# Optimization experiments

Measured on AMD Instinct MI355X. Metric: run time of the kernel, lower is better.

The kernel has to match this reference:

```python
import jax, jax.numpy as jnp
import numpy as np

EPS = 1e-6
SCALE = 1.0
GRID_HEIGHT = 4.0
GRID_RES_Y = 1.0


def _perspective(mat, vec):
    # mat [3,4], vec [...,3] -> (points [...,2], flag [...,3])
    homog = jnp.einsum('ij,...j->...i', mat[:, :3], vec) + mat[:, 3]
    pos = homog[..., 2:3] > 0
    flag = jnp.concatenate([pos, pos, jnp.ones_like(pos)], axis=-1).astype(homog.dtype)
    homog = homog * flag  # zero x,y behind camera; z kept (flag[...,-1]=True)
    return homog[..., :2] / homog[..., 2:3], flag


def _fisheye(pts, k, D, flag):
    cx, cy, fx, fy = k[0, 2], k[1, 2], k[0, 0], k[1, 1]
    x = (pts[..., 0] - cx) / fx
    y = (pts[..., 1] - cy) / fy
    r = jnp.sqrt(x * x + y * y)
    th = jnp.arctan(r)
    t2 = th * th
    rad = th * (1 + D[0] * t2 + D[1] * t2 ** 2 + D[2] * t2 ** 3 + D[5] * t2 ** 4) / r
    xd = x * rad * fx + cx
    yd = y * rad * fy + cy
    return jnp.stack([xd, yd], axis=-1) * flag[..., :2]


def _pinhole(pts, k, D, flag):
    cx, cy, fx, fy = k[0, 2], k[1, 2], k[0, 0], k[1, 1]
    x = (pts[..., 0] - cx) / fx
    y = (pts[..., 1] - cy) / fy
    k1, k2, k3, p1, p2 = D[0], D[1], D[2], D[3], D[4]
    r2 = x * x + y * y
    poly = 1 + k1 * r2 + k2 * r2 * r2 + k3 * r2 * r2 * r2
    xd = x * poly + (2 * p1 * x * y + p2 * (r2 + 2 * x * x))
    yd = y * poly + (p1 * (r2 + 2 * y * y) + 2 * p2 * x * y)
    return jnp.stack([xd * fx + cx, yd * fy + cy], axis=-1) * flag[..., :2]


def _bilinear(img, coords):
    # torch F.grid_sample(align_corners=True, padding_mode='border'); img [C,H,W], coords [...,2] in [-1,1]
    C, H, W = img.shape
    x = jnp.clip((coords[..., 0] + 1) * 0.5 * (W - 1), 0.0, W - 1)
    y = jnp.clip((coords[..., 1] + 1) * 0.5 * (H - 1), 0.0, H - 1)
    x0 = jnp.floor(x)
    y0 = jnp.floor(y)
    wx = x - x0
    wy = y - y0
    x0i = x0.astype(jnp.int32)
    y0i = y0.astype(jnp.int32)
    x1i = jnp.minimum(x0i + 1, W - 1)
    y1i = jnp.minimum(y0i + 1, H - 1)
    flat = img.reshape(C, H * W)

    def g(yi, xi):
        return jnp.take(flat, (yi * W + xi).reshape(-1), axis=1).reshape((C,) + coords.shape[:-1])

    v00 = g(y0i, x0i)
    v01 = g(y0i, x1i)
    v10 = g(y1i, x0i)
    v11 = g(y1i, x1i)
    return v00 * (1 - wx) * (1 - wy) + v01 * wx * (1 - wy) + v10 * (1 - wx) * wy + v11 * wx * wy


def _per_image(feature, k, imu2c, post_rot, post_tran, undist, corner):
    C, Hf, Wf = feature.shape
    calib = k @ imu2c                                  # [3,4]
    pts, flag = _perspective(calib, corner)            # pts [Ny,Zd,Xd,2]
    pts = jnp.where(undist[-1] == 1,
                    _fisheye(pts, k, undist, flag),
                    _pinhole(pts, k, undist, flag))
    pts = jnp.einsum('ij,...j->...i', post_rot[:2, :2], pts) + post_tran[:2]
    nc = jnp.clip(2.0 * (pts / SCALE) - 1.0, -1.0, 1.0)  # [Ny,Zd,Xd,2]
    s0, s1 = slice(None, -1), slice(1, None)
    # 8 voxel corners -> [8, Ny-1, D, Wd, 2]
    corners8 = jnp.stack([nc[a, b, c] for a in (s0, s1) for b in (s0, s1) for c in (s0, s1)], axis=0)
    left = corners8[..., 0].min(0)
    right = corners8[..., 0].max(0)
    top = corners8[..., 1].min(0)
    bot = corners8[..., 1].max(0)
    Nh, D, Wd = left.shape
    bbox = jnp.stack([left, top, right, bot], axis=-1).reshape(Nh, D * Wd, 4)
    area = (bbox[..., 2] - bbox[..., 0]) * (bbox[..., 3] - bbox[..., 1]) * Hf * Wf * 0.25 + EPS  # [Nh,P]
    integ = jnp.cumsum(jnp.cumsum(feature, axis=-1), axis=-2)  # integral image [C,Hf,Wf]
    tl = _bilinear(integ, bbox[..., 0:2])
    br = _bilinear(integ, bbox[..., 2:4])
    tr = _bilinear(integ, jnp.stack([bbox[..., 2], bbox[..., 1]], axis=-1))
    bl = _bilinear(integ, jnp.stack([bbox[..., 0], bbox[..., 3]], axis=-1))
    vox = (tl + br - tr - bl) / area * (area > EPS)    # [C,Nh,P]
    return vox.reshape(C * Nh, D, Wd)                  # neck == '2d'


def _forward(features, ks, imu2cs, post_rots, post_trans, undists, grid):
    ys = -jnp.arange(0.0, GRID_HEIGHT, GRID_RES_Y) + GRID_HEIGHT / 2.0
    y_corners = jnp.stack([jnp.zeros_like(ys), ys, jnp.zeros_like(ys)], axis=-1)  # [Ny,3]
    corners = grid[:, None] + y_corners[None, :, None, None, :]                   # [B,Ny,Zd,Xd,3]
    per_cam = jax.vmap(_per_image, in_axes=(0, 0, 0, 0, 0, 0, None))

    def per_batch(f, k, m, pr, pt, ud, c):
        # drop_idx = [] -> all cameras kept; max over cameras
        return per_cam(f, k, m, pr, pt, ud, c).max(axis=0)

    return jax.vmap(per_batch)(features, ks, imu2cs, post_rots, post_trans, undists, corners)


def setup_inputs():
    key = jax.random.key(0)
    B, N, C, Hf, Wf = 1, 6, 64, 64, 176
    Zd = Xd = 129
    kf, ku = jax.random.split(key, 2)
    features = jax.random.normal(kf, (B, N, C, Hf, Wf), jnp.float32)
    # intrinsics (realistic pinhole values keep the projection numerically sane)
    K = np.zeros((B, N, 3, 3), np.float32)
    K[..., 0, 0] = 600.0
    K[..., 1, 1] = 600.0
    K[..., 0, 2] = 704.0
    K[..., 1, 2] = 256.0
    K[..., 2, 2] = 1.0
    ks = jnp.asarray(K)
    # extrinsics: per-camera yaw + small translation
    m = np.zeros((B, N, 3, 4), np.float32)
    for i in range(N):
        th = 0.25 * (i - 2.5)
        R = np.array([[np.cos(th), 0.0, np.sin(th)],
                      [0.0, 1.0, 0.0],
                      [-np.sin(th), 0.0, np.cos(th)]], np.float32)
        m[:, i, :, :3] = R
        m[:, i, :, 3] = np.array([0.1 * i, -1.5, 0.2], np.float32)
    imu2cs = jnp.asarray(m)
    pr = np.zeros((B, N, 3, 3), np.float32)
    pr[..., 0, 0] = 1.0 / 1408.0
    pr[..., 1, 1] = 1.0 / 512.0
    pr[..., 2, 2] = 1.0
    post_rots = jnp.asarray(pr)
    post_trans = jnp.zeros((B, N, 3), jnp.float32)
    und = 0.01 * np.array(jax.random.normal(ku, (B, N, 7)), np.float32)
    und[..., 6] = 0.0
    und[:, :3, 6] = 1.0  # first 3 cameras fisheye, rest pinhole
    undists = jnp.asarray(und)
    x = np.linspace(-40.0, 40.0, Xd, dtype=np.float32)
    z = np.linspace(3.0, 80.0, Zd, dtype=np.float32)
    zz, xx = np.meshgrid(z, x, indexing='ij')
    g = np.stack([xx, np.zeros_like(xx), zz], axis=-1)[None]  # [1,Zd,Xd,3]
    grid = jnp.asarray(np.broadcast_to(g, (B, Zd, Xd, 3)).copy())
    return {"features": features, "ks": ks, "imu2cs": imu2cs, "post_rots": post_rots,
            "post_trans": post_trans, "undists": undists, "grid": grid}


def reference(features, ks, imu2cs, post_rots, post_trans, undists, grid):
    return _forward(features, ks, imu2cs, post_rots, post_trans, undists, grid)
```

## Files before the change

kernel.cpp:

```cpp
#include <hip/hip_runtime.h>
#include <math.h>

#define NCAM 6
#define C_CH 64
#define HF   64
#define WF   176
#define GDIM 129
#define NY   4
#define NH   3
#define DD   128
#define WDIM 128
#define NP   (DD*WDIM)

struct alignas(16) BoxP {
    int   oTL, oTR, oBL, oBR;
    float wxL, wxR, wyT, wyB;
    float area;
    int   pad0, pad1, pad2;
};
static_assert(sizeof(BoxP) == 48, "BoxP size");

__device__ __forceinline__ int rfl_i(int x) {
    return __builtin_amdgcn_readfirstlane(x);
}
__device__ __forceinline__ float rfl_f(float x) {
    return __builtin_bit_cast(float, __builtin_amdgcn_readfirstlane(__builtin_bit_cast(int, x)));
}

__global__ void k_project(const float* __restrict__ ks,
                          const float* __restrict__ imu2cs,
                          const float* __restrict__ post_rots,
                          const float* __restrict__ post_trans,
                          const float* __restrict__ undists,
                          const float* __restrict__ grid,
                          float2* __restrict__ ncbuf)
{
    const int n   = blockIdx.y;
    const int idx = blockIdx.x * blockDim.x + threadIdx.x;
    const int per = NY * GDIM * GDIM;
    if (idx >= per) return;
    const int ny  = idx / (GDIM * GDIM);
    const int rem = idx % (GDIM * GDIM);
    const int gz  = rem / GDIM;
    const int gx  = rem % GDIM;

    const float* k  = ks         + n * 9;
    const float* m  = imu2cs     + n * 12;
    const float* pr = post_rots  + n * 9;
    const float* pt = post_trans + n * 3;
    const float* D  = undists    + n * 7;

    float cal[12];
    #pragma unroll
    for (int i = 0; i < 3; ++i)
        #pragma unroll
        for (int j = 0; j < 4; ++j)
            cal[i*4+j] = k[i*3+0]*m[0*4+j] + k[i*3+1]*m[1*4+j] + k[i*3+2]*m[2*4+j];

    const float vx = grid[(gz*GDIM + gx)*3 + 0];
    const float vy = 2.0f - (float)ny;
    const float vz = grid[(gz*GDIM + gx)*3 + 2];

    const float hx = cal[0]*vx + cal[1]*vy + cal[2]*vz  + cal[3];
    const float hy = cal[4]*vx + cal[5]*vy + cal[6]*vz  + cal[7];
    const float hz = cal[8]*vx + cal[9]*vy + cal[10]*vz + cal[11];

    const float fl = (hz > 0.0f) ? 1.0f : 0.0f;
    const float px = (hx * fl) / hz;
    const float py = (hy * fl) / hz;

    const float fx = k[0], fy = k[4], cx = k[2], cy = k[5];
    const float x = (px - cx) / fx;
    const float y = (py - cy) / fy;

    float xd, yd;
    if (D[6] == 1.0f) {
        const float r  = sqrtf(x*x + y*y);
        const float th = atanf(r);
        const float t2 = th * th;
        const float t4 = t2 * t2;
        const float rad = th * (1.0f + D[0]*t2 + D[1]*t4 + D[2]*(t2*t4) + D[5]*(t4*t4)) / r;
        xd = x * rad * fx + cx;
        yd = y * rad * fy + cy;
    } else {
        const float k1 = D[0], k2 = D[1], k3 = D[2], p1 = D[3], p2 = D[4];
        const float r2 = x*x + y*y;
        const float poly = 1.0f + k1*r2 + k2*r2*r2 + k3*r2*r2*r2;
        const float xdd = x*poly + (2.0f*p1*x*y + p2*(r2 + 2.0f*x*x));
        const float ydd = y*poly + (p1*(r2 + 2.0f*y*y) + 2.0f*p2*x*y);
        xd = xdd * fx + cx;
        yd = ydd * fy + cy;
    }
    xd *= fl; yd *= fl;

    const float qx = pr[0]*xd + pr[1]*yd + pt[0];
    const float qy = pr[3]*xd + pr[4]*yd + pt[1];
    const float ncx = fminf(fmaxf(2.0f*qx - 1.0f, -1.0f), 1.0f);
    const float ncy = fminf(fmaxf(2.0f*qy - 1.0f, -1.0f), 1.0f);
    ncbuf[((n*NY + ny)*GDIM + gz)*GDIM + gx] = make_float2(ncx, ncy);
}

__global__ __launch_bounds__(256) void k_rowcum(const float* __restrict__ feat,
                                                float* __restrict__ rowsum)
{
    __shared__ float T[WF * 65];
    __shared__ float S[4][C_CH];
    __shared__ float OFF[4][C_CH];
    const int h   = blockIdx.x;
    const int n   = blockIdx.y;
    const int tid = threadIdx.x;

    for (int idx = tid; idx < C_CH * WF; idx += 256) {
        const int cc = idx / WF;
        const int w  = idx % WF;
        T[w*65 + cc] = feat[((size_t)(n*C_CH + cc)*HF + h)*WF + w];
    }
    __syncthreads();
    {
        const int cc = tid & 63, seg = tid >> 6;
        const int w0 = seg * 44;
        float run = 0.0f;
        #pragma unroll
        for (int i = 0; i < 44; ++i) {
            run += T[(w0 + i)*65 + cc];
            T[(w0 + i)*65 + cc] = run;
        }
        S[seg][cc] = run;
    }
    __syncthreads();
    {
        const int cc = tid & 63, seg = tid >> 6;
        float off = 0.0f;
        #pragma unroll
        for (int s = 0; s < 3; ++s)
            if (s < seg) off += S[s][cc];
        OFF[seg][cc] = off;
    }
    __syncthreads();
    float* outp = rowsum + (size_t)(n*HF + h) * (WF * C_CH);
    for (int idx = tid; idx < WF * C_CH; idx += 256) {
        const int w  = idx >> 6;
        const int cc = idx & 63;
        outp[idx] = T[w*65 + cc] + OFF[w/44][cc];
    }
}

__global__ __launch_bounds__(256) void k_quadcol(const float* __restrict__ rowsum,
                                                 float4* __restrict__ qbuf)
{
    __shared__ float A[HF][C_CH];
    __shared__ float Bb[HF][C_CH];
    __shared__ float tA[4][C_CH], tB[4][C_CH];
    const int x  = blockIdx.x;
    const int n  = blockIdx.y;
    const int x1 = min(x + 1, WF - 1);
    const int c  = threadIdx.x & 63;
    const int hq = threadIdx.x >> 6;

    const float* base0 = rowsum + (size_t)n*HF*WF*C_CH + (size_t)x  * C_CH + c;
    const float* base1 = rowsum + (size_t)n*HF*WF*C_CH + (size_t)x1 * C_CH + c;
    float run0 = 0.0f, run1 = 0.0f;
    #pragma unroll
    for (int i = 0; i < 16; ++i) {
        const int h = hq*16 + i;
        run0 += base0[(size_t)h * (WF*C_CH)];
        run1 += base1[(size_t)h * (WF*C_CH)];
        A[h][c]  = run0;
        Bb[h][c] = run1;
    }
    tA[hq][c] = run0;
    tB[hq][c] = run1;
    __syncthreads();
    {
        float offA = 0.0f, offB = 0.0f;
        #pragma unroll
        for (int s = 0; s < 3; ++s)
            if (s < hq) { offA += tA[s][c]; offB += tB[s][c]; }
        #pragma unroll
        for (int i = 0; i < 16; ++i) {
            const int h = hq*16 + i;
            A[h][c]  += offA;
            Bb[h][c] += offB;
        }
    }
    __syncthreads();
    float4* qb = qbuf + ((size_t)n*HF*WF + x) * C_CH + c;
    #pragma unroll
    for (int i = 0; i < 16; ++i) {
        const int h  = hq*16 + i;
        const int hn = min(h + 1, HF - 1);
        float4 q;
        q.x = A[h][c];  q.y = Bb[h][c];
        q.z = A[hn][c]; q.w = Bb[hn][c];
        qb[(size_t)h * (WF*C_CH)] = q;
    }
}

__global__ void k_boxparams(const float2* __restrict__ ncbuf, BoxP* __restrict__ bp)
{
    const int idx = blockIdx.x * blockDim.x + threadIdx.x;
    if (idx >= NCAM * NH * NP) return;
    const int n  = idx / (NH * NP);
    const int r  = idx % (NH * NP);
    const int nh = r / NP;
    const int p  = r % NP;
    const int d  = p / WDIM;
    const int wd = p % WDIM;

    float left = 1e30f, right = -1e30f, top = 1e30f, bot = -1e30f;
    #pragma unroll
    for (int a = 0; a < 2; ++a)
        #pragma unroll
        for (int b = 0; b < 2; ++b)
            #pragma unroll
            for (int cc = 0; cc < 2; ++cc) {
                const float2 v = ncbuf[((n*NY + nh + a)*GDIM + d + b)*GDIM + wd + cc];
                left  = fminf(left,  v.x);  right = fmaxf(right, v.x);
                top   = fminf(top,   v.y);  bot   = fmaxf(bot,   v.y);
            }

    const float area = (right - left) * (bot - top) * (float)HF * (float)WF * 0.25f + 1e-6f;

    const float xLp = fminf(fmaxf((left  + 1.0f) * 0.5f * (float)(WF-1), 0.0f), (float)(WF-1));
    const float xRp = fminf(fmaxf((right + 1.0f) * 0.5f * (float)(WF-1), 0.0f), (float)(WF-1));
    const float yTp = fminf(fmaxf((top   + 1.0f) * 0.5f * (float)(HF-1), 0.0f), (float)(HF-1));
    const float yBp = fminf(fmaxf((bot   + 1.0f) * 0.5f * (float)(HF-1), 0.0f), (float)(HF-1));
    const float xL0 = floorf(xLp), xR0 = floorf(xRp), yT0 = floorf(yTp), yB0 = floorf(yBp);

    const int rT = (int)yT0 * (WF*C_CH*16);
    const int rB = (int)yB0 * (WF*C_CH*16);
    const int cL = (int)xL0 * (C_CH*16);
    const int cR = (int)xR0 * (C_CH*16);

    BoxP o;
    o.oTL = rT + cL; o.oTR = rT + cR; o.oBL = rB + cL; o.oBR = rB + cR;
    o.wxL = xLp - xL0; o.wxR = xRp - xR0; o.wyT = yTp - yT0; o.wyB = yBp - yB0;
    o.area = area; o.pad0 = 0; o.pad1 = 0; o.pad2 = 0;
    bp[idx] = o;
}

__global__ __launch_bounds__(256) void k_sample(const float4* __restrict__ qbuf,
                                                const BoxP* __restrict__ bp,
                                                float* __restrict__ out)
{
    __shared__ float sm[C_CH][33];
    const int nh   = blockIdx.y;
    const int p0   = blockIdx.x * 32;
    const int tid  = threadIdx.x;
    const int wave = __builtin_amdgcn_readfirstlane(tid >> 6);
    const int c    = tid & 63;

    #pragma unroll 1
    for (int j = 0; j < 8; ++j) {
        const int pj = p0 + wave*8 + j;
        float vmax = -3.402823466e38f;
        #pragma unroll 1
        for (int n = 0; n < NCAM; ++n) {
            const BoxP* bpp = &bp[(n*NH + nh)*NP + pj];
            const float area = rfl_f(bpp->area);
            if (!(area > 1e-6f)) {
                vmax = fmaxf(vmax, 0.0f);
                continue;
            }
            const int oTL = rfl_i(bpp->oTL), oTR = rfl_i(bpp->oTR);
            const int oBL = rfl_i(bpp->oBL), oBR = rfl_i(bpp->oBR);
            const float wxL = rfl_f(bpp->wxL), wxR = rfl_f(bpp->wxR);
            const float wyT = rfl_f(bpp->wyT), wyB = rfl_f(bpp->wyB);

            const char* qb = (const char*)qbuf + (size_t)n * ((size_t)HF*WF*C_CH*16);
            auto LDQ = [&](int off) -> float4 {
                return ((const float4*)(qb + (size_t)off))[c];
            };
            const float4 qTL = LDQ(oTL);
            const float4 qTR = LDQ(oTR);
            const float4 qBL = LDQ(oBL);
            const float4 qBR = LDQ(oBR);

            auto BIL = [&](const float4& q, float wx, float wy) -> float {
                const float m0 = fmaf(wx, q.y - q.x, q.x);
                const float m1 = fmaf(wx, q.w - q.z, q.z);
                return fmaf(wy, m1 - m0, m0);
            };
            const float tl = BIL(qTL, wxL, wyT);
            const float tr = BIL(qTR, wxR, wyT);
            const float bl = BIL(qBL, wxL, wyB);
            const float br = BIL(qBR, wxR, wyB);
            const float s  = (tl + br) - (tr + bl);
            vmax = fmaxf(vmax, s * __builtin_amdgcn_rcpf(area));
        }
        sm[c][wave*8 + j] = vmax;
    }
    __syncthreads();
    for (int idx = tid; idx < C_CH * 32; idx += 256) {
        const int cc = idx >> 5;
        const int jj = idx & 31;
        out[(size_t)(cc*NH + nh)*NP + p0 + jj] = sm[cc][jj];
    }
}

extern "C" void kernel_launch(void* const* d_in, const int* in_sizes, int n_in,
                              void* d_out, int out_size, void* d_ws, size_t ws_size,
                              hipStream_t stream)
{
    const float* feats      = (const float*)d_in[0];
    const float* ks         = (const float*)d_in[1];
    const float* imu2cs     = (const float*)d_in[2];
    const float* post_rots  = (const float*)d_in[3];
    const float* post_trans = (const float*)d_in[4];
    const float* undists    = (const float*)d_in[5];
    const float* grid       = (const float*)d_in[6];
    float* out = (float*)d_out;

    char* ws = (char*)d_ws;
    size_t off = 0;
    float2* ncbuf = (float2*)(ws + off);
    off += sizeof(float2) * NCAM * NY * GDIM * GDIM;
    off = (off + 255) & ~(size_t)255;
    float* rowsum = (float*)(ws + off);
    off += sizeof(float) * NCAM * HF * WF * C_CH;
    off = (off + 255) & ~(size_t)255;
    float4* qbuf = (float4*)(ws + off);
    off += sizeof(float4) * (size_t)NCAM * HF * WF * C_CH;
    off = (off + 255) & ~(size_t)255;
    BoxP* bp = (BoxP*)(ws + off);
    off += sizeof(BoxP) * NCAM * NH * NP;
    (void)ws_size; (void)in_sizes; (void)n_in; (void)out_size;

    dim3 g1((NY*GDIM*GDIM + 255)/256, NCAM);
    k_project<<<g1, 256, 0, stream>>>(ks, imu2cs, post_rots, post_trans, undists, grid, ncbuf);

    dim3 g2a(HF, NCAM);
    k_rowcum<<<g2a, 256, 0, stream>>>(feats, rowsum);

    dim3 g2b(WF, NCAM);
    k_quadcol<<<g2b, 256, 0, stream>>>(rowsum, qbuf);

    dim3 g3((NCAM*NH*NP + 255)/256);
    k_boxparams<<<g3, 256, 0, stream>>>(ncbuf, bp);

    dim3 g4(NP/32, NH);
    k_sample<<<g4, 256, 0, stream>>>(qbuf, bp, out);
}
```

Before: 158.0 us.

## Fuse projection into box-param kernel, register-scan quadcol, unroll camera loop

Removes the separate projection kernel and its ncbuf buffer, recomputing the eight corner projections inline in the box-parameter kernel, which saves a launch and a round trip through global memory. In exchange each grid point is projected up to 8 times, including atan and division work. The column-scan kernel now keeps prefix sums in registers instead of shared arrays and drops one barrier. The sampling kernel fully unrolls the camera loop and replaces the early-continue with a select, so the loads can be issued together, at the cost of also loading for degenerate boxes.

```diff
diff --git a/kernel.cpp b/kernel.cpp
--- a/kernel.cpp
+++ b/kernel.cpp
@@ -27,79 +27,6 @@
     return __builtin_bit_cast(float, __builtin_amdgcn_readfirstlane(__builtin_bit_cast(int, x)));
 }
 
-__global__ void k_project(const float* __restrict__ ks,
-                          const float* __restrict__ imu2cs,
-                          const float* __restrict__ post_rots,
-                          const float* __restrict__ post_trans,
-                          const float* __restrict__ undists,
-                          const float* __restrict__ grid,
-                          float2* __restrict__ ncbuf)
-{
-    const int n   = blockIdx.y;
-    const int idx = blockIdx.x * blockDim.x + threadIdx.x;
-    const int per = NY * GDIM * GDIM;
-    if (idx >= per) return;
-    const int ny  = idx / (GDIM * GDIM);
-    const int rem = idx % (GDIM * GDIM);
-    const int gz  = rem / GDIM;
-    const int gx  = rem % GDIM;
-
-    const float* k  = ks         + n * 9;
-    const float* m  = imu2cs     + n * 12;
-    const float* pr = post_rots  + n * 9;
-    const float* pt = post_trans + n * 3;
-    const float* D  = undists    + n * 7;
-
-    float cal[12];
-    #pragma unroll
-    for (int i = 0; i < 3; ++i)
-        #pragma unroll
-        for (int j = 0; j < 4; ++j)
-            cal[i*4+j] = k[i*3+0]*m[0*4+j] + k[i*3+1]*m[1*4+j] + k[i*3+2]*m[2*4+j];
-
-    const float vx = grid[(gz*GDIM + gx)*3 + 0];
-    const float vy = 2.0f - (float)ny;
-    const float vz = grid[(gz*GDIM + gx)*3 + 2];
-
-    const float hx = cal[0]*vx + cal[1]*vy + cal[2]*vz  + cal[3];
-    const float hy = cal[4]*vx + cal[5]*vy + cal[6]*vz  + cal[7];
-    const float hz = cal[8]*vx + cal[9]*vy + cal[10]*vz + cal[11];
-
-    const float fl = (hz > 0.0f) ? 1.0f : 0.0f;
-    const float px = (hx * fl) / hz;
-    const float py = (hy * fl) / hz;
-
-    const float fx = k[0], fy = k[4], cx = k[2], cy = k[5];
-    const float x = (px - cx) / fx;
-    const float y = (py - cy) / fy;
-
-    float xd, yd;
-    if (D[6] == 1.0f) {
-        const float r  = sqrtf(x*x + y*y);
-        const float th = atanf(r);
-        const float t2 = th * th;
-        const float t4 = t2 * t2;
-        const float rad = th * (1.0f + D[0]*t2 + D[1]*t4 + D[2]*(t2*t4) + D[5]*(t4*t4)) / r;
-        xd = x * rad * fx + cx;
-        yd = y * rad * fy + cy;
-    } else {
-        const float k1 = D[0], k2 = D[1], k3 = D[2], p1 = D[3], p2 = D[4];
-        const float r2 = x*x + y*y;
-        const float poly = 1.0f + k1*r2 + k2*r2*r2 + k3*r2*r2*r2;
-        const float xdd = x*poly + (2.0f*p1*x*y + p2*(r2 + 2.0f*x*x));
-        const float ydd = y*poly + (p1*(r2 + 2.0f*y*y) + 2.0f*p2*x*y);
-        xd = xdd * fx + cx;
-        yd = ydd * fy + cy;
-    }
-    xd *= fl; yd *= fl;
-
-    const float qx = pr[0]*xd + pr[1]*yd + pt[0];
-    const float qy = pr[3]*xd + pr[4]*yd + pt[1];
-    const float ncx = fminf(fmaxf(2.0f*qx - 1.0f, -1.0f), 1.0f);
-    const float ncy = fminf(fmaxf(2.0f*qy - 1.0f, -1.0f), 1.0f);
-    ncbuf[((n*NY + ny)*GDIM + gz)*GDIM + gx] = make_float2(ncx, ncy);
-}
-
 __global__ __launch_bounds__(256) void k_rowcum(const float* __restrict__ feat,
                                                 float* __restrict__ rowsum)
 {
@@ -148,9 +75,8 @@
 __global__ __launch_bounds__(256) void k_quadcol(const float* __restrict__ rowsum,
                                                  float4* __restrict__ qbuf)
 {
-    __shared__ float A[HF][C_CH];
-    __shared__ float Bb[HF][C_CH];
     __shared__ float tA[4][C_CH], tB[4][C_CH];
+    __shared__ float fA[4][C_CH], fB[4][C_CH];
     const int x  = blockIdx.x;
     const int n  = blockIdx.y;
     const int x1 = min(x + 1, WF - 1);
@@ -159,44 +85,64 @@
 
     const float* base0 = rowsum + (size_t)n*HF*WF*C_CH + (size_t)x  * C_CH + c;
     const float* base1 = rowsum + (size_t)n*HF*WF*C_CH + (size_t)x1 * C_CH + c;
-    float run0 = 0.0f, run1 = 0.0f;
+
+    float eA[16], eB[16];
     #pragma unroll
     for (int i = 0; i < 16; ++i) {
         const int h = hq*16 + i;
-        run0 += base0[(size_t)h * (WF*C_CH)];
-        run1 += base1[(size_t)h * (WF*C_CH)];
-        A[h][c]  = run0;
-        Bb[h][c] = run1;
-    }
-    tA[hq][c] = run0;
-    tB[hq][c] = run1;
-    __syncthreads();
-    {
-        float offA = 0.0f, offB = 0.0f;
-        #pragma unroll
-        for (int s = 0; s < 3; ++s)
-            if (s < hq) { offA += tA[s][c]; offB += tB[s][c]; }
-        #pragma unroll
-        for (int i = 0; i < 16; ++i) {
-            const int h = hq*16 + i;
-            A[h][c]  += offA;
-            Bb[h][c] += offB;
+        eA[i] = base0[(size_t)h * (WF*C_CH)];
+        eB[i] = base1[(size_t)h * (WF*C_CH)];
+    }
+    float sA[16], sB[16];
+    sA[0] = eA[0]; sB[0] = eB[0];
+    #pragma unroll
+    for (int i = 1; i < 16; ++i) {
+        sA[i] = sA[i-1] + eA[i];
+        sB[i] = sB[i-1] + eB[i];
+    }
+    tA[hq][c] = sA[15]; tB[hq][c] = sB[15];
+    fA[hq][c] = eA[0];  fB[hq][c] = eB[0];
+    __syncthreads();
+
+    float offA = 0.0f, offB = 0.0f;
+    #pragma unroll
+    for (int s = 0; s < 3; ++s)
+        if (s < hq) { offA += tA[s][c]; offB += tB[s][c]; }
+
+    float nextA, nextB;
+    if (hq < 3) {
+        nextA = fA[hq+1][c] + (offA + tA[hq][c]);
+        nextB = fB[hq+1][c] + (offB + tB[hq][c]);
+    } else {
+        nextA = sA[15] + offA;
+        nextB = sB[15] + offB;
+    }
+
+    float4* qb = qbuf + ((size_t)n*HF*WF + x) * C_CH + c;
+    #pragma unroll
+    for (int i = 0; i < 16; ++i) {
+        const int h = hq*16 + i;
+        float4 q;
+        q.x = sA[i] + offA;
+        q.y = sB[i] + offB;
+        if (i < 15) {
+            q.z = sA[i+1] + offA;
+            q.w = sB[i+1] + offB;
+        } else {
+            q.z = nextA;
+            q.w = nextB;
         }
-    }
-    __syncthreads();
-    float4* qb = qbuf + ((size_t)n*HF*WF + x) * C_CH + c;
-    #pragma unroll
-    for (int i = 0; i < 16; ++i) {
-        const int h  = hq*16 + i;
-        const int hn = min(h + 1, HF - 1);
-        float4 q;
-        q.x = A[h][c];  q.y = Bb[h][c];
-        q.z = A[hn][c]; q.w = Bb[hn][c];
         qb[(size_t)h * (WF*C_CH)] = q;
     }
 }
 
-__global__ void k_boxparams(const float2* __restrict__ ncbuf, BoxP* __restrict__ bp)
+__global__ void k_boxproj(const float* __restrict__ ks,
+                          const float* __restrict__ imu2cs,
+                          const float* __restrict__ post_rots,
+                          const float* __restrict__ post_trans,
+                          const float* __restrict__ undists,
+                          const float* __restrict__ grid,
+                          BoxP* __restrict__ bp)
 {
     const int idx = blockIdx.x * blockDim.x + threadIdx.x;
     if (idx >= NCAM * NH * NP) return;
@@ -207,17 +153,75 @@
     const int d  = p / WDIM;
     const int wd = p % WDIM;
 
+    const float* k  = ks         + n * 9;
+    const float* m  = imu2cs     + n * 12;
+    const float* pr = post_rots  + n * 9;
+    const float* pt = post_trans + n * 3;
+    const float* D  = undists    + n * 7;
+
+    float cal[12];
+    #pragma unroll
+    for (int i = 0; i < 3; ++i)
+        #pragma unroll
+        for (int j = 0; j < 4; ++j)
+            cal[i*4+j] = k[i*3+0]*m[0*4+j] + k[i*3+1]*m[1*4+j] + k[i*3+2]*m[2*4+j];
+
+    const float fx = k[0], fy = k[4], cx = k[2], cy = k[5];
+    const bool fish = (D[6] == 1.0f);
+    const float D0 = D[0], D1 = D[1], D2 = D[2], D3 = D[3], D4 = D[4], D5 = D[5];
+
     float left = 1e30f, right = -1e30f, top = 1e30f, bot = -1e30f;
     #pragma unroll
-    for (int a = 0; a < 2; ++a)
-        #pragma unroll
-        for (int b = 0; b < 2; ++b)
+    for (int a = 0; a < 2; ++a) {
+        const float vy = 2.0f - (float)(nh + a);
+        #pragma unroll
+        for (int b = 0; b < 2; ++b) {
             #pragma unroll
             for (int cc = 0; cc < 2; ++cc) {
-                const float2 v = ncbuf[((n*NY + nh + a)*GDIM + d + b)*GDIM + wd + cc];
-                left  = fminf(left,  v.x);  right = fmaxf(right, v.x);
-                top   = fminf(top,   v.y);  bot   = fmaxf(bot,   v.y);
+                const int gz = d + b, gx = wd + cc;
+                const float vx = grid[(gz*GDIM + gx)*3 + 0];
+                const float vz = grid[(gz*GDIM + gx)*3 + 2];
+
+                const float hx = cal[0]*vx + cal[1]*vy + cal[2]*vz  + cal[3];
+                const float hy = cal[4]*vx + cal[5]*vy + cal[6]*vz  + cal[7];
+                const float hz = cal[8]*vx + cal[9]*vy + cal[10]*vz + cal[11];
+
+                const float fl = (hz > 0.0f) ? 1.0f : 0.0f;
+                const float px = (hx * fl) / hz;
+                const float py = (hy * fl) / hz;
+
+                const float x = (px - cx) / fx;
+                const float y = (py - cy) / fy;
+
+                float xd, yd;
+                if (fish) {
+                    const float rr = sqrtf(x*x + y*y);
+                    const float th = atanf(rr);
+                    const float t2 = th * th;
+                    const float t4 = t2 * t2;
+                    const float rad = th * (1.0f + D0*t2 + D1*t4 + D2*(t2*t4) + D5*(t4*t4)) / rr;
+                    xd = x * rad * fx + cx;
+                    yd = y * rad * fy + cy;
+                } else {
+                    const float r2 = x*x + y*y;
+                    const float poly = 1.0f + D0*r2 + D1*r2*r2 + D2*r2*r2*r2;
+                    const float xdd = x*poly + (2.0f*D3*x*y + D4*(r2 + 2.0f*x*x));
+                    const float ydd = y*poly + (D3*(r2 + 2.0f*y*y) + 2.0f*D4*x*y);
+                    xd = xdd * fx + cx;
+                    yd = ydd * fy + cy;
+                }
+                xd *= fl; yd *= fl;
+
+                const float qx = pr[0]*xd + pr[1]*yd + pt[0];
+                const float qy = pr[3]*xd + pr[4]*yd + pt[1];
+                const float ncx = fminf(fmaxf(2.0f*qx - 1.0f, -1.0f), 1.0f);
+                const float ncy = fminf(fmaxf(2.0f*qy - 1.0f, -1.0f), 1.0f);
+
+                left  = fminf(left,  ncx);  right = fmaxf(right, ncx);
+                top   = fminf(top,   ncy);  bot   = fmaxf(bot,   ncy);
             }
+        }
+    }
 
     const float area = (right - left) * (bot - top) * (float)HF * (float)WF * 0.25f + 1e-6f;
 
@@ -253,28 +257,22 @@
     #pragma unroll 1
     for (int j = 0; j < 8; ++j) {
         const int pj = p0 + wave*8 + j;
+        const BoxP* bb = bp + nh*NP + pj;
         float vmax = -3.402823466e38f;
-        #pragma unroll 1
+        #pragma unroll
         for (int n = 0; n < NCAM; ++n) {
-            const BoxP* bpp = &bp[(n*NH + nh)*NP + pj];
+            const BoxP* bpp = bb + n * (NH*NP);
             const float area = rfl_f(bpp->area);
-            if (!(area > 1e-6f)) {
-                vmax = fmaxf(vmax, 0.0f);
-                continue;
-            }
             const int oTL = rfl_i(bpp->oTL), oTR = rfl_i(bpp->oTR);
             const int oBL = rfl_i(bpp->oBL), oBR = rfl_i(bpp->oBR);
             const float wxL = rfl_f(bpp->wxL), wxR = rfl_f(bpp->wxR);
             const float wyT = rfl_f(bpp->wyT), wyB = rfl_f(bpp->wyB);
 
             const char* qb = (const char*)qbuf + (size_t)n * ((size_t)HF*WF*C_CH*16);
-            auto LDQ = [&](int off) -> float4 {
-                return ((const float4*)(qb + (size_t)off))[c];
-            };
-            const float4 qTL = LDQ(oTL);
-            const float4 qTR = LDQ(oTR);
-            const float4 qBL = LDQ(oBL);
-            const float4 qBR = LDQ(oBR);
+            const float4 qTL = ((const float4*)(qb + (size_t)oTL))[c];
+            const float4 qTR = ((const float4*)(qb + (size_t)oTR))[c];
+            const float4 qBL = ((const float4*)(qb + (size_t)oBL))[c];
+            const float4 qBR = ((const float4*)(qb + (size_t)oBR))[c];
 
             auto BIL = [&](const float4& q, float wx, float wy) -> float {
                 const float m0 = fmaf(wx, q.y - q.x, q.x);
@@ -286,7 +284,9 @@
             const float bl = BIL(qBL, wxL, wyB);
             const float br = BIL(qBR, wxR, wyB);
             const float s  = (tl + br) - (tr + bl);
-            vmax = fmaxf(vmax, s * __builtin_amdgcn_rcpf(area));
+            float v = s * __builtin_amdgcn_rcpf(area);
+            v = (area > 1e-6f) ? v : 0.0f;
+            vmax = fmaxf(vmax, v);
         }
         sm[c][wave*8 + j] = vmax;
     }
@@ -313,9 +313,6 @@
 
     char* ws = (char*)d_ws;
     size_t off = 0;
-    float2* ncbuf = (float2*)(ws + off);
-    off += sizeof(float2) * NCAM * NY * GDIM * GDIM;
-    off = (off + 255) & ~(size_t)255;
     float* rowsum = (float*)(ws + off);
     off += sizeof(float) * NCAM * HF * WF * C_CH;
     off = (off + 255) & ~(size_t)255;
@@ -326,17 +323,14 @@
     off += sizeof(BoxP) * NCAM * NH * NP;
     (void)ws_size; (void)in_sizes; (void)n_in; (void)out_size;
 
-    dim3 g1((NY*GDIM*GDIM + 255)/256, NCAM);
-    k_project<<<g1, 256, 0, stream>>>(ks, imu2cs, post_rots, post_trans, undists, grid, ncbuf);
-
-    dim3 g2a(HF, NCAM);
-    k_rowcum<<<g2a, 256, 0, stream>>>(feats, rowsum);
-
-    dim3 g2b(WF, NCAM);
-    k_quadcol<<<g2b, 256, 0, stream>>>(rowsum, qbuf);
+    dim3 g1(HF, NCAM);
+    k_rowcum<<<g1, 256, 0, stream>>>(feats, rowsum);
+
+    dim3 g2(WF, NCAM);
+    k_quadcol<<<g2, 256, 0, stream>>>(rowsum, qbuf);
 
     dim3 g3((NCAM*NH*NP + 255)/256);
-    k_boxparams<<<g3, 256, 0, stream>>>(ncbuf, bp);
+    k_boxproj<<<g3, 256, 0, stream>>>(ks, imu2cs, post_rots, post_trans, undists, grid, bp);
 
     dim3 g4(NP/32, NH);
     k_sample<<<g4, 256, 0, stream>>>(qbuf, bp, out);
```

Result: slower. 162.6 us (+2.9%).
